# Kernel tuning notes

Hardware: AMD Instinct MI355X
Metric: run time of the kernel (lower is better)

## Reference

```python
import jax, jax.numpy as jnp
import numpy as np

S, B, F, H, K = 256, 2048, 5, 64, 8  # seq, batch, feat, hidden, num aux inputs


def setup_inputs() -> dict:
    key = jax.random.key(0)
    ks = jax.random.split(key, 20)
    def rn(k, shape, s=1.0):
        return jax.random.normal(k, shape, dtype=jnp.float32) * s
    inp = {}
    names = ["Y"] + ["x%d" % i for i in range(1, 9)]
    for i, nm in enumerate(names):
        inp[nm] = rn(ks[i], (S, B, F))
    p = 0.1  # weight scale for stability
    inp["W_main"] = rn(ks[9], (F, 4 * H), p)   # main-input proj for gates [i,f,o,c]
    inp["U_main"] = rn(ks[10], (H, 4 * H), p)
    inp["b_main"] = jnp.zeros((4 * H,), jnp.float32)
    inp["W_aux"] = rn(ks[11], (K, F, 2 * H), p)  # per-aux proj for [i_k, c_k]
    inp["U_aux"] = rn(ks[12], (K, H, 2 * H), p)
    inp["b_aux"] = jnp.zeros((K, 2 * H), jnp.float32)
    inp["W_att"] = rn(ks[13], (H, H), p)        # attention bilinear form vs C_{t-1}
    inp["b_att"] = jnp.zeros((1,), jnp.float32)
    inp["W_ih"] = rn(ks[14], (4 * H, H), p)     # standard LSTM (torch gate order i,f,g,o)
    inp["W_hh"] = rn(ks[15], (4 * H, H), p)
    inp["b_ih"] = jnp.zeros((4 * H,), jnp.float32)
    inp["b_hh"] = jnp.zeros((4 * H,), jnp.float32)
    inp["lin_W"] = rn(ks[16], (1, H), p)
    inp["lin_b"] = jnp.zeros((1,), jnp.float32)
    return inp


def _forward(Y, x1, x2, x3, x4, x5, x6, x7, x8,
             W_main, U_main, b_main, W_aux, U_aux, b_aux, W_att, b_att,
             W_ih, W_hh, b_ih, b_hh, lin_W, lin_b):
    Hd = U_main.shape[0]
    X = jnp.stack([x1, x2, x3, x4, x5, x6, x7, x8], axis=2)  # (S,B,K,F)
    Bsz = Y.shape[1]
    h0 = jnp.zeros((Bsz, Hd), Y.dtype)
    c0 = jnp.zeros((Bsz, Hd), Y.dtype)

    def mi_step(carry, t):
        h, c = carry
        yt, xt = t  # (B,F), (B,K,F)
        gm = yt @ W_main + h @ U_main + b_main  # (B,4H)
        i = jax.nn.sigmoid(gm[:, :Hd])
        f = jax.nn.sigmoid(gm[:, Hd:2 * Hd])
        o = jax.nn.sigmoid(gm[:, 2 * Hd:3 * Hd])
        cm = jnp.tanh(gm[:, 3 * Hd:])
        ga = (jnp.einsum('bkf,kfg->bkg', xt, W_aux)
              + jnp.einsum('bh,khg->bkg', h, U_aux) + b_aux)  # (B,K,2H)
        ik = jax.nn.sigmoid(ga[..., :Hd])
        ck = jnp.tanh(ga[..., Hd:])
        # candidate contributions: main + each auxiliary -> (B,K+1,H)
        l = jnp.concatenate([(i * cm)[:, None, :], ik * ck], axis=1)
        # attention of each candidate against previous cell state
        u = jnp.tanh(jnp.einsum('bkh,hg,bg->bk', l, W_att, c) + b_att)  # (B,K+1)
        a = jax.nn.softmax(u, axis=-1)
        L = jnp.einsum('bk,bkh->bh', a, l)
        c_new = f * c + L
        h_new = o * jnp.tanh(c_new)
        return (h_new, c_new), h_new

    _, hs = jax.lax.scan(mi_step, (h0, c0), (Y, X))  # hs: (S,B,H)

    # standard LSTM over the MI-LSTM hidden sequence
    pre = hs @ W_ih.T + (b_ih + b_hh)  # (S,B,4H)

    def lstm_step(carry, g_in):
        h, c = carry
        g = g_in + h @ W_hh.T
        i = jax.nn.sigmoid(g[:, :Hd])
        f = jax.nn.sigmoid(g[:, Hd:2 * Hd])
        gg = jnp.tanh(g[:, 2 * Hd:3 * Hd])
        o = jax.nn.sigmoid(g[:, 3 * Hd:])
        c = f * c + i * gg
        h = o * jnp.tanh(c)
        return (h, c), h

    _, outs = jax.lax.scan(lstm_step, (h0, c0), pre)  # (S,B,H)
    return jax.nn.relu(outs) @ lin_W.T + lin_b  # (S,B,1)


def reference(Y, x1, x2, x3, x4, x5, x6, x7, x8,
              W_main, U_main, b_main, W_aux, U_aux, b_aux, W_att, b_att,
              W_ih, W_hh, b_ih, b_hh, lin_W, lin_b):
    return _forward(Y, x1, x2, x3, x4, x5, x6, x7, x8,
                    W_main, U_main, b_main, W_aux, U_aux, b_aux, W_att, b_att,
                    W_ih, W_hh, b_ih, b_hh, lin_W, lin_b)
```

## Files before the change

kernel.cpp:

```cpp
#include <hip/hip_runtime.h>
#include <cstddef>
#include <math.h>

#define SEQ   256
#define BATCH 2048
#define FD    5
#define HD    64
#define KAUX  8
#define NCOL  1280
#define ROWS  8
#define NTHR  256

__device__ __forceinline__ float sigm(float x) { return 1.0f / (1.0f + expf(-x)); }
__device__ __forceinline__ float tanh_f(float x) { return tanhf(x); }

__device__ __forceinline__ float wave_sum(float v) {
#pragma unroll
    for (int m = 1; m < 64; m <<= 1) v += __shfl_xor(v, m);
    return v;
}

__global__ __launch_bounds__(NTHR, 1)
void minet_fused(const float* __restrict__ Y,
                 const float* __restrict__ x1, const float* __restrict__ x2,
                 const float* __restrict__ x3, const float* __restrict__ x4,
                 const float* __restrict__ x5, const float* __restrict__ x6,
                 const float* __restrict__ x7, const float* __restrict__ x8,
                 const float* __restrict__ W_main, const float* __restrict__ U_main,
                 const float* __restrict__ b_main, const float* __restrict__ W_aux,
                 const float* __restrict__ U_aux,  const float* __restrict__ b_aux,
                 const float* __restrict__ W_att,  const float* __restrict__ b_att,
                 const float* __restrict__ W_ih,   const float* __restrict__ W_hh,
                 const float* __restrict__ b_ih,   const float* __restrict__ b_hh,
                 const float* __restrict__ lin_W,  const float* __restrict__ lin_b,
                 float* __restrict__ out)
{
    __shared__ __align__(16) float h1[ROWS][HD];
    __shared__ __align__(16) float c1[ROWS][HD];
    __shared__ __align__(16) float h2[ROWS][HD];
    __shared__ __align__(16) float outb[ROWS][NCOL];
    __shared__ __align__(16) float outg[2][ROWS][256];
    __shared__ __align__(16) float inb[ROWS][9][8];
    __shared__ __align__(16) float WaT[HD * HD];

    const int tid  = threadIdx.x;
    const int lane = tid & 63;
    const int wid  = tid >> 6;
    const int b0   = blockIdx.x * ROWS;

    for (int i = tid; i < HD * HD; i += NTHR) {
        int g = i >> 6, h = i & 63;
        WaT[i] = W_att[h * 64 + g];
    }

    const float* uptr[5];
    float wf[5][5];
    float bias[5];
    int   inoff[5];
#pragma unroll
    for (int j = 0; j < 5; ++j) {
        if (j == 0) {
            uptr[0] = U_main + tid;
#pragma unroll
            for (int f = 0; f < FD; ++f) wf[0][f] = W_main[f * 256 + tid];
            bias[0]  = b_main[tid];
            inoff[0] = 0;
        } else {
            int c  = tid + 256 * j - 256;
            int kk = c >> 7, gg = c & 127;
            uptr[j] = U_aux + (size_t)kk * 64 * 128 + gg;
#pragma unroll
            for (int f = 0; f < FD; ++f) wf[j][f] = W_aux[(kk * 5 + f) * 128 + gg];
            bias[j]  = b_aux[kk * 128 + gg];
            inoff[j] = (1 + kk) * 8;
        }
    }

    const float* wsrc = (tid < 128) ? W_ih : W_hh;
    const int cc = tid & 127;
    float4 w2v[2][16];
#pragma unroll
    for (int j2 = 0; j2 < 2; ++j2)
#pragma unroll
        for (int hb = 0; hb < 16; ++hb)
            w2v[j2][hb] = *(const float4*)(wsrc + (size_t)(cc + 128 * j2) * 64 + hb * 4);
    float bias2[2];
#pragma unroll
    for (int j2 = 0; j2 < 2; ++j2)
        bias2[j2] = (tid < 128) ? (b_ih[cc + 128 * j2] + b_hh[cc + 128 * j2]) : 0.0f;

    const float linw = lin_W[lane];
    const float linb = lin_b[0];
    const float batt = b_att[0];

    for (int i = tid; i < ROWS * HD; i += NTHR) {
        (&h1[0][0])[i] = 0.0f; (&c1[0][0])[i] = 0.0f; (&h2[0][0])[i] = 0.0f;
    }
    for (int i = tid; i < ROWS * 9 * 8; i += NTHR) (&inb[0][0][0])[i] = 0.0f;
    float c2r[2] = {0.0f, 0.0f};

    bool  pon[2]; const float* psrc[2]; int pofs[2]; float pf[2];
#pragma unroll
    for (int q = 0; q < 2; ++q) {
        int idx = tid + 256 * q;
        pon[q] = idx < 360;
        int r = idx / 45, rem = idx % 45;
        int s = rem / 5, f = rem % 5;
        const float* base = Y;
        if (s == 1) base = x1; else if (s == 2) base = x2; else if (s == 3) base = x3;
        else if (s == 4) base = x4; else if (s == 5) base = x5; else if (s == 6) base = x6;
        else if (s == 7) base = x7; else if (s == 8) base = x8;
        psrc[q] = base + (size_t)(b0 + r) * FD + f;
        pofs[q] = (r * 9 + s) * 8 + f;
        pf[q] = 0.0f;
        if (pon[q]) pf[q] = psrc[q][0];
    }

    const int r0 = wid * 2;

    for (int t = 0; t < SEQ; ++t) {
#pragma unroll
        for (int q = 0; q < 2; ++q)
            if (pon[q]) (&inb[0][0][0])[pofs[q]] = pf[q];
        __syncthreads();

        if (t + 1 < SEQ) {
#pragma unroll
            for (int q = 0; q < 2; ++q)
                if (pon[q]) pf[q] = psrc[q][(size_t)(t + 1) * BATCH * FD];
        }

        float acc[5][ROWS];
#pragma unroll
        for (int j = 0; j < 5; ++j) {
#pragma unroll
            for (int r = 0; r < ROWS; ++r) {
                const float* ip = &inb[r][0][0] + inoff[j];
                float4 ia = *(const float4*)ip;
                float  i4 = ip[4];
                acc[j][r] = bias[j] + ia.x * wf[j][0] + ia.y * wf[j][1] + ia.z * wf[j][2]
                                    + ia.w * wf[j][3] + i4 * wf[j][4];
            }
        }
        {
            const float* up[5];
#pragma unroll
            for (int j = 0; j < 5; ++j) up[j] = uptr[j];
#pragma unroll 2
            for (int hb = 0; hb < 16; ++hb) {
                float s4a[ROWS][4];
#pragma unroll
                for (int r = 0; r < ROWS; ++r) {
                    float4 f4 = *(const float4*)&h1[r][hb * 4];
                    s4a[r][0] = f4.x; s4a[r][1] = f4.y; s4a[r][2] = f4.z; s4a[r][3] = f4.w;
                }
#pragma unroll
                for (int hi = 0; hi < 4; ++hi) {
                    float w[5];
#pragma unroll
                    for (int j = 0; j < 5; ++j)
                        w[j] = up[j][(size_t)hi * (j == 0 ? 256 : 128)];
#pragma unroll
                    for (int j = 0; j < 5; ++j)
#pragma unroll
                        for (int r = 0; r < ROWS; ++r)
                            acc[j][r] = fmaf(s4a[r][hi], w[j], acc[j][r]);
                }
#pragma unroll
                for (int j = 0; j < 5; ++j) up[j] += 4 * (j == 0 ? 256 : 128);
            }
        }
#pragma unroll
        for (int j = 0; j < 5; ++j)
#pragma unroll
            for (int r = 0; r < ROWS; ++r)
                outb[r][tid + 256 * j] = acc[j][r];

        float v0 = 0.0f, v1 = 0.0f;
        {
            float cr0 = c1[r0][lane];
            float cr1 = c1[r0 + 1][lane];
#pragma unroll
            for (int g = 0; g < 64; ++g) {
                float w = WaT[g * 64 + lane];
                v0 = fmaf(__shfl(cr0, g), w, v0);
                v1 = fmaf(__shfl(cr1, g), w, v1);
            }
        }
        __syncthreads();

#pragma unroll
        for (int rr = 0; rr < 2; ++rr) {
            const int r = r0 + rr;
            const float vv = rr ? v1 : v0;
            float gi = outb[r][lane],       gf = outb[r][64 + lane];
            float go = outb[r][128 + lane], gc = outb[r][192 + lane];
            float ii = sigm(gi), ff = sigm(gf), oo = sigm(go), cm = tanh_f(gc);
            float l[9];
            l[0] = ii * cm;
#pragma unroll
            for (int k = 1; k <= 8; ++k) {
                float a_ = outb[r][256 + (k - 1) * 128 + lane];
                float b_ = outb[r][256 + (k - 1) * 128 + 64 + lane];
                l[k] = sigm(a_) * tanh_f(b_);
            }
            float u[9]; float umax = -1e30f;
#pragma unroll
            for (int k = 0; k < 9; ++k) {
                float p = wave_sum(l[k] * vv);
                u[k] = tanh_f(p + batt);
                umax = fmaxf(umax, u[k]);
            }
            float den = 0.0f, Lh = 0.0f;
#pragma unroll
            for (int k = 0; k < 9; ++k) {
                float e = expf(u[k] - umax);
                den += e;
                Lh = fmaf(e, l[k], Lh);
            }
            Lh /= den;
            float cp = c1[r][lane];
            float cn = fmaf(ff, cp, Lh);
            float hn = oo * tanh_f(cn);
            c1[r][lane] = cn;
            h1[r][lane] = hn;
        }
        __syncthreads();

        {
            float acc2[2][ROWS];
#pragma unroll
            for (int j2 = 0; j2 < 2; ++j2)
#pragma unroll
                for (int r = 0; r < ROWS; ++r) acc2[j2][r] = bias2[j2];
            const float(*SS)[HD] = (tid < 128) ? h1 : h2;
#pragma unroll
            for (int hb = 0; hb < 16; ++hb) {
                float s4a[ROWS][4];
#pragma unroll
                for (int r = 0; r < ROWS; ++r) {
                    float4 f4 = *(const float4*)&SS[r][hb * 4];
                    s4a[r][0] = f4.x; s4a[r][1] = f4.y; s4a[r][2] = f4.z; s4a[r][3] = f4.w;
                }
#pragma unroll
                for (int j2 = 0; j2 < 2; ++j2) {
                    float4 w4 = w2v[j2][hb];
#pragma unroll
                    for (int r = 0; r < ROWS; ++r)
                        acc2[j2][r] = fmaf(s4a[r][0], w4.x,
                                      fmaf(s4a[r][1], w4.y,
                                      fmaf(s4a[r][2], w4.z,
                                      fmaf(s4a[r][3], w4.w, acc2[j2][r]))));
                }
            }
            const int part = (tid < 128) ? 0 : 1;
#pragma unroll
            for (int j2 = 0; j2 < 2; ++j2)
#pragma unroll
                for (int r = 0; r < ROWS; ++r)
                    outg[part][r][cc + 128 * j2] = acc2[j2][r];
        }
        __syncthreads();

#pragma unroll
        for (int rr = 0; rr < 2; ++rr) {
            const int r = r0 + rr;
            float g0 = outg[0][r][lane]       + outg[1][r][lane];
            float g1 = outg[0][r][64 + lane]  + outg[1][r][64 + lane];
            float g2 = outg[0][r][128 + lane] + outg[1][r][128 + lane];
            float g3 = outg[0][r][192 + lane] + outg[1][r][192 + lane];
            float i2 = sigm(g0), f2 = sigm(g1), gg = tanh_f(g2), o2 = sigm(g3);
            float cn = fmaf(f2, c2r[rr], i2 * gg);
            c2r[rr] = cn;
            float hn = o2 * tanh_f(cn);
            h2[r][lane] = hn;
            float e = wave_sum(fmaxf(hn, 0.0f) * linw);
            if (lane == 0) out[(size_t)t * BATCH + b0 + r] = e + linb;
        }
    }
}

extern "C" void kernel_launch(void* const* d_in, const int* in_sizes, int n_in,
                              void* d_out, int out_size, void* d_ws, size_t ws_size,
                              hipStream_t stream) {
    const float* Y      = (const float*)d_in[0];
    const float* x1     = (const float*)d_in[1];
    const float* x2     = (const float*)d_in[2];
    const float* x3     = (const float*)d_in[3];
    const float* x4     = (const float*)d_in[4];
    const float* x5     = (const float*)d_in[5];
    const float* x6     = (const float*)d_in[6];
    const float* x7     = (const float*)d_in[7];
    const float* x8     = (const float*)d_in[8];
    const float* W_main = (const float*)d_in[9];
    const float* U_main = (const float*)d_in[10];
    const float* b_main = (const float*)d_in[11];
    const float* W_aux  = (const float*)d_in[12];
    const float* U_aux  = (const float*)d_in[13];
    const float* b_aux  = (const float*)d_in[14];
    const float* W_att  = (const float*)d_in[15];
    const float* b_att  = (const float*)d_in[16];
    const float* W_ih   = (const float*)d_in[17];
    const float* W_hh   = (const float*)d_in[18];
    const float* b_ih   = (const float*)d_in[19];
    const float* b_hh   = (const float*)d_in[20];
    const float* lin_W  = (const float*)d_in[21];
    const float* lin_b  = (const float*)d_in[22];
    float* out = (float*)d_out;

    dim3 grid(BATCH / ROWS);
    dim3 block(NTHR);
    minet_fused<<<grid, block, 0, stream>>>(Y, x1, x2, x3, x4, x5, x6, x7, x8,
                                            W_main, U_main, b_main, W_aux, U_aux, b_aux,
                                            W_att, b_att, W_ih, W_hh, b_ih, b_hh,
                                            lin_W, lin_b, out);
}
```

Baseline: 7.468 ms.

## Double threads per block and transpose U weights for contiguous float4 column loads

Raises the block size from 256 to 512 threads so each thread computes 2-3 gate columns instead of 5, and each wave handles one batch row in the elementwise phases instead of two. A small pre-kernel transposes U_main and U_aux into a column-major workspace so each thread reads its weight column as contiguous float4 loads. The second LSTM's weights are now streamed from global memory on every step instead of being held in registers. The intent is more latency hiding per step of the sequential recurrence, at the cost of an extra launch, uneven work between threads (only half have a third column), and repeated per-step global weight traffic.

After: 25.95 ms. 248% more time.

```diff
diff --git a/kernel.cpp b/kernel.cpp
--- a/kernel.cpp
+++ b/kernel.cpp
@@ -6,10 +6,9 @@
 #define BATCH 2048
 #define FD    5
 #define HD    64
-#define KAUX  8
 #define NCOL  1280
 #define ROWS  8
-#define NTHR  256
+#define NTHR  512
 
 __device__ __forceinline__ float sigm(float x) { return 1.0f / (1.0f + expf(-x)); }
 __device__ __forceinline__ float tanh_f(float x) { return tanhf(x); }
@@ -20,15 +19,30 @@
     return v;
 }
 
-__global__ __launch_bounds__(NTHR, 1)
+__global__ void transpose_u(const float* __restrict__ U_main,
+                            const float* __restrict__ U_aux,
+                            float* __restrict__ Ut) {
+    const int c = blockIdx.x;
+    const int h = threadIdx.x;
+    float v;
+    if (c < 256) {
+        v = U_main[h * 256 + c];
+    } else {
+        int cp = c - 256, kk = cp >> 7, gg = cp & 127;
+        v = U_aux[(size_t)kk * 64 * 128 + h * 128 + gg];
+    }
+    Ut[c * 64 + h] = v;
+}
+
+__global__ __launch_bounds__(NTHR, 2)
 void minet_fused(const float* __restrict__ Y,
                  const float* __restrict__ x1, const float* __restrict__ x2,
                  const float* __restrict__ x3, const float* __restrict__ x4,
                  const float* __restrict__ x5, const float* __restrict__ x6,
                  const float* __restrict__ x7, const float* __restrict__ x8,
-                 const float* __restrict__ W_main, const float* __restrict__ U_main,
+                 const float* __restrict__ W_main, const float* __restrict__ Ut,
                  const float* __restrict__ b_main, const float* __restrict__ W_aux,
-                 const float* __restrict__ U_aux,  const float* __restrict__ b_aux,
+                 const float* __restrict__ b_aux,
                  const float* __restrict__ W_att,  const float* __restrict__ b_att,
                  const float* __restrict__ W_ih,   const float* __restrict__ W_hh,
                  const float* __restrict__ b_ih,   const float* __restrict__ b_hh,
@@ -47,47 +61,47 @@
     const int lane = tid & 63;
     const int wid  = tid >> 6;
     const int b0   = blockIdx.x * ROWS;
+    const bool has3 = (tid < 256);
 
     for (int i = tid; i < HD * HD; i += NTHR) {
         int g = i >> 6, h = i & 63;
         WaT[i] = W_att[h * 64 + g];
     }
 
-    const float* uptr[5];
-    float wf[5][5];
-    float bias[5];
-    int   inoff[5];
-#pragma unroll
-    for (int j = 0; j < 5; ++j) {
-        if (j == 0) {
-            uptr[0] = U_main + tid;
-#pragma unroll
-            for (int f = 0; f < FD; ++f) wf[0][f] = W_main[f * 256 + tid];
-            bias[0]  = b_main[tid];
-            inoff[0] = 0;
+    int colv[3];
+    colv[0] = tid; colv[1] = tid + 512; colv[2] = has3 ? tid + 1024 : 0;
+    float wf[3][5];
+    float bias[3];
+    int   inoff[3];
+    const float* utp[3];
+#pragma unroll
+    for (int j = 0; j < 3; ++j) {
+        if (j < 2 || has3) {
+            int c = colv[j];
+            utp[j] = Ut + (size_t)c * 64;
+            if (c < 256) {
+#pragma unroll
+                for (int f = 0; f < FD; ++f) wf[j][f] = W_main[f * 256 + c];
+                bias[j]  = b_main[c];
+                inoff[j] = 0;
+            } else {
+                int cp = c - 256, kk = cp >> 7, gg = cp & 127;
+#pragma unroll
+                for (int f = 0; f < FD; ++f) wf[j][f] = W_aux[(kk * 5 + f) * 128 + gg];
+                bias[j]  = b_aux[kk * 128 + gg];
+                inoff[j] = (1 + kk) * 8;
+            }
         } else {
-            int c  = tid + 256 * j - 256;
-            int kk = c >> 7, gg = c & 127;
-            uptr[j] = U_aux + (size_t)kk * 64 * 128 + gg;
-#pragma unroll
-            for (int f = 0; f < FD; ++f) wf[j][f] = W_aux[(kk * 5 + f) * 128 + gg];
-            bias[j]  = b_aux[kk * 128 + gg];
-            inoff[j] = (1 + kk) * 8;
-        }
-    }
-
-    const float* wsrc = (tid < 128) ? W_ih : W_hh;
-    const int cc = tid & 127;
-    float4 w2v[2][16];
-#pragma unroll
-    for (int j2 = 0; j2 < 2; ++j2)
-#pragma unroll
-        for (int hb = 0; hb < 16; ++hb)
-            w2v[j2][hb] = *(const float4*)(wsrc + (size_t)(cc + 128 * j2) * 64 + hb * 4);
-    float bias2[2];
-#pragma unroll
-    for (int j2 = 0; j2 < 2; ++j2)
-        bias2[j2] = (tid < 128) ? (b_ih[cc + 128 * j2] + b_hh[cc + 128 * j2]) : 0.0f;
+            utp[j] = Ut; bias[j] = 0.0f; inoff[j] = 0;
+#pragma unroll
+            for (int f = 0; f < FD; ++f) wf[j][f] = 0.0f;
+        }
+    }
+
+    const int  cc      = tid & 255;
+    const bool ispart1 = (tid >= 256);
+    const float* wcol  = (ispart1 ? W_hh : W_ih) + (size_t)cc * 64;
+    const float  b2    = ispart1 ? 0.0f : (b_ih[cc] + b_hh[cc]);
 
     const float linw = lin_W[lane];
     const float linb = lin_b[0];
@@ -97,102 +111,89 @@
         (&h1[0][0])[i] = 0.0f; (&c1[0][0])[i] = 0.0f; (&h2[0][0])[i] = 0.0f;
     }
     for (int i = tid; i < ROWS * 9 * 8; i += NTHR) (&inb[0][0][0])[i] = 0.0f;
-    float c2r[2] = {0.0f, 0.0f};
-
-    bool  pon[2]; const float* psrc[2]; int pofs[2]; float pf[2];
-#pragma unroll
-    for (int q = 0; q < 2; ++q) {
-        int idx = tid + 256 * q;
-        pon[q] = idx < 360;
-        int r = idx / 45, rem = idx % 45;
+    float c2 = 0.0f;
+
+    const bool pon = (tid < 360);
+    const float* psrc = Y;
+    int pofs = 0;
+    float pf = 0.0f;
+    if (pon) {
+        int r = tid / 45, rem = tid % 45;
         int s = rem / 5, f = rem % 5;
         const float* base = Y;
         if (s == 1) base = x1; else if (s == 2) base = x2; else if (s == 3) base = x3;
         else if (s == 4) base = x4; else if (s == 5) base = x5; else if (s == 6) base = x6;
         else if (s == 7) base = x7; else if (s == 8) base = x8;
-        psrc[q] = base + (size_t)(b0 + r) * FD + f;
-        pofs[q] = (r * 9 + s) * 8 + f;
-        pf[q] = 0.0f;
-        if (pon[q]) pf[q] = psrc[q][0];
-    }
-
-    const int r0 = wid * 2;
+        psrc = base + (size_t)(b0 + r) * FD + f;
+        pofs = (r * 9 + s) * 8 + f;
+        pf   = psrc[0];
+    }
 
     for (int t = 0; t < SEQ; ++t) {
-#pragma unroll
-        for (int q = 0; q < 2; ++q)
-            if (pon[q]) (&inb[0][0][0])[pofs[q]] = pf[q];
+        if (pon) (&inb[0][0][0])[pofs] = pf;
         __syncthreads();
 
-        if (t + 1 < SEQ) {
-#pragma unroll
-            for (int q = 0; q < 2; ++q)
-                if (pon[q]) pf[q] = psrc[q][(size_t)(t + 1) * BATCH * FD];
-        }
-
-        float acc[5][ROWS];
-#pragma unroll
-        for (int j = 0; j < 5; ++j) {
-#pragma unroll
-            for (int r = 0; r < ROWS; ++r) {
-                const float* ip = &inb[r][0][0] + inoff[j];
-                float4 ia = *(const float4*)ip;
-                float  i4 = ip[4];
-                acc[j][r] = bias[j] + ia.x * wf[j][0] + ia.y * wf[j][1] + ia.z * wf[j][2]
-                                    + ia.w * wf[j][3] + i4 * wf[j][4];
-            }
-        }
+        if (pon && t + 1 < SEQ) pf = psrc[(size_t)(t + 1) * BATCH * FD];
+
+        float acc[3][ROWS];
+#pragma unroll
+        for (int j = 0; j < 3; ++j) {
+            if (j < 2 || has3) {
+#pragma unroll
+                for (int r = 0; r < ROWS; ++r) {
+                    const float* ip = &inb[r][0][0] + inoff[j];
+                    float4 ia = *(const float4*)ip;
+                    float  i4 = ip[4];
+                    acc[j][r] = bias[j] + ia.x * wf[j][0] + ia.y * wf[j][1] + ia.z * wf[j][2]
+                                        + ia.w * wf[j][3] + i4 * wf[j][4];
+                }
+            }
+        }
+#pragma unroll 4
+        for (int hb = 0; hb < 16; ++hb) {
+            float4 hreg[ROWS];
+#pragma unroll
+            for (int r = 0; r < ROWS; ++r) hreg[r] = *(const float4*)&h1[r][hb * 4];
+            float4 w0 = *(const float4*)(utp[0] + hb * 4);
+            float4 w1 = *(const float4*)(utp[1] + hb * 4);
+#pragma unroll
+            for (int r = 0; r < ROWS; ++r)
+                acc[0][r] = fmaf(hreg[r].x, w0.x, fmaf(hreg[r].y, w0.y,
+                            fmaf(hreg[r].z, w0.z, fmaf(hreg[r].w, w0.w, acc[0][r]))));
+#pragma unroll
+            for (int r = 0; r < ROWS; ++r)
+                acc[1][r] = fmaf(hreg[r].x, w1.x, fmaf(hreg[r].y, w1.y,
+                            fmaf(hreg[r].z, w1.z, fmaf(hreg[r].w, w1.w, acc[1][r]))));
+            if (has3) {
+                float4 w2 = *(const float4*)(utp[2] + hb * 4);
+#pragma unroll
+                for (int r = 0; r < ROWS; ++r)
+                    acc[2][r] = fmaf(hreg[r].x, w2.x, fmaf(hreg[r].y, w2.y,
+                                fmaf(hreg[r].z, w2.z, fmaf(hreg[r].w, w2.w, acc[2][r]))));
+            }
+        }
+#pragma unroll
+        for (int j = 0; j < 3; ++j) {
+            if (j < 2 || has3) {
+#pragma unroll
+                for (int r = 0; r < ROWS; ++r)
+                    outb[r][colv[j]] = acc[j][r];
+            }
+        }
+
+        float v0 = 0.0f;
         {
-            const float* up[5];
-#pragma unroll
-            for (int j = 0; j < 5; ++j) up[j] = uptr[j];
-#pragma unroll 2
-            for (int hb = 0; hb < 16; ++hb) {
-                float s4a[ROWS][4];
-#pragma unroll
-                for (int r = 0; r < ROWS; ++r) {
-                    float4 f4 = *(const float4*)&h1[r][hb * 4];
-                    s4a[r][0] = f4.x; s4a[r][1] = f4.y; s4a[r][2] = f4.z; s4a[r][3] = f4.w;
-                }
-#pragma unroll
-                for (int hi = 0; hi < 4; ++hi) {
-                    float w[5];
-#pragma unroll
-                    for (int j = 0; j < 5; ++j)
-                        w[j] = up[j][(size_t)hi * (j == 0 ? 256 : 128)];
-#pragma unroll
-                    for (int j = 0; j < 5; ++j)
-#pragma unroll
-                        for (int r = 0; r < ROWS; ++r)
-                            acc[j][r] = fmaf(s4a[r][hi], w[j], acc[j][r]);
-                }
-#pragma unroll
-                for (int j = 0; j < 5; ++j) up[j] += 4 * (j == 0 ? 256 : 128);
-            }
-        }
-#pragma unroll
-        for (int j = 0; j < 5; ++j)
-#pragma unroll
-            for (int r = 0; r < ROWS; ++r)
-                outb[r][tid + 256 * j] = acc[j][r];
-
-        float v0 = 0.0f, v1 = 0.0f;
-        {
-            float cr0 = c1[r0][lane];
-            float cr1 = c1[r0 + 1][lane];
+            float cr0 = c1[wid][lane];
 #pragma unroll
             for (int g = 0; g < 64; ++g) {
                 float w = WaT[g * 64 + lane];
                 v0 = fmaf(__shfl(cr0, g), w, v0);
-                v1 = fmaf(__shfl(cr1, g), w, v1);
             }
         }
         __syncthreads();
 
-#pragma unroll
-        for (int rr = 0; rr < 2; ++rr) {
-            const int r = r0 + rr;
-            const float vv = rr ? v1 : v0;
+        {
+            const int r = wid;
             float gi = outb[r][lane],       gf = outb[r][64 + lane];
             float go = outb[r][128 + lane], gc = outb[r][192 + lane];
             float ii = sigm(gi), ff = sigm(gf), oo = sigm(go), cm = tanh_f(gc);
@@ -207,7 +208,7 @@
             float u[9]; float umax = -1e30f;
 #pragma unroll
             for (int k = 0; k < 9; ++k) {
-                float p = wave_sum(l[k] * vv);
+                float p = wave_sum(l[k] * v0);
                 u[k] = tanh_f(p + batt);
                 umax = fmaxf(umax, u[k]);
             }
@@ -228,50 +229,35 @@
         __syncthreads();
 
         {
-            float acc2[2][ROWS];
-#pragma unroll
-            for (int j2 = 0; j2 < 2; ++j2)
-#pragma unroll
-                for (int r = 0; r < ROWS; ++r) acc2[j2][r] = bias2[j2];
-            const float(*SS)[HD] = (tid < 128) ? h1 : h2;
-#pragma unroll
+            float accg[ROWS];
+#pragma unroll
+            for (int r = 0; r < ROWS; ++r) accg[r] = b2;
+            const float(*SS)[HD] = ispart1 ? h2 : h1;
+#pragma unroll 4
             for (int hb = 0; hb < 16; ++hb) {
-                float s4a[ROWS][4];
+                float4 w4 = *(const float4*)(wcol + hb * 4);
 #pragma unroll
                 for (int r = 0; r < ROWS; ++r) {
-                    float4 f4 = *(const float4*)&SS[r][hb * 4];
-                    s4a[r][0] = f4.x; s4a[r][1] = f4.y; s4a[r][2] = f4.z; s4a[r][3] = f4.w;
+                    float4 s4 = *(const float4*)&SS[r][hb * 4];
+                    accg[r] = fmaf(s4.x, w4.x, fmaf(s4.y, w4.y,
+                              fmaf(s4.z, w4.z, fmaf(s4.w, w4.w, accg[r]))));
                 }
-#pragma unroll
-                for (int j2 = 0; j2 < 2; ++j2) {
-                    float4 w4 = w2v[j2][hb];
-#pragma unroll
-                    for (int r = 0; r < ROWS; ++r)
-                        acc2[j2][r] = fmaf(s4a[r][0], w4.x,
-                                      fmaf(s4a[r][1], w4.y,
-                                      fmaf(s4a[r][2], w4.z,
-                                      fmaf(s4a[r][3], w4.w, acc2[j2][r]))));
-                }
-            }
-            const int part = (tid < 128) ? 0 : 1;
-#pragma unroll
-            for (int j2 = 0; j2 < 2; ++j2)
-#pragma unroll
-                for (int r = 0; r < ROWS; ++r)
-                    outg[part][r][cc + 128 * j2] = acc2[j2][r];
+            }
+#pragma unroll
+            for (int r = 0; r < ROWS; ++r)
+                outg[ispart1 ? 1 : 0][r][cc] = accg[r];
         }
         __syncthreads();
 
-#pragma unroll
-        for (int rr = 0; rr < 2; ++rr) {
-            const int r = r0 + rr;
+        {
+            const int r = wid;
             float g0 = outg[0][r][lane]       + outg[1][r][lane];
             float g1 = outg[0][r][64 + lane]  + outg[1][r][64 + lane];
             float g2 = outg[0][r][128 + lane] + outg[1][r][128 + lane];
             float g3 = outg[0][r][192 + lane] + outg[1][r][192 + lane];
             float i2 = sigm(g0), f2 = sigm(g1), gg = tanh_f(g2), o2 = sigm(g3);
-            float cn = fmaf(f2, c2r[rr], i2 * gg);
-            c2r[rr] = cn;
+            float cn = fmaf(f2, c2, i2 * gg);
+            c2 = cn;
             float hn = o2 * tanh_f(cn);
             h2[r][lane] = hn;
             float e = wave_sum(fmaxf(hn, 0.0f) * linw);
@@ -307,11 +293,14 @@
     const float* lin_W  = (const float*)d_in[21];
     const float* lin_b  = (const float*)d_in[22];
     float* out = (float*)d_out;
+    float* Ut  = (float*)d_ws;
+
+    transpose_u<<<dim3(NCOL), dim3(HD), 0, stream>>>(U_main, U_aux, Ut);
 
     dim3 grid(BATCH / ROWS);
     dim3 block(NTHR);
     minet_fused<<<grid, block, 0, stream>>>(Y, x1, x2, x3, x4, x5, x6, x7, x8,
-                                            W_main, U_main, b_main, W_aux, U_aux, b_aux,
+                                            W_main, Ut, b_main, W_aux, b_aux,
                                             W_att, b_att, W_ih, W_hh, b_ih, b_hh,
                                             lin_W, lin_b, out);
 }
```
